# Optimization experiments

Hardware: AMD Instinct MI355X
Metric: run time of the kernel (lower is better)

## Reference

```python
import jax, jax.numpy as jnp
import numpy as np
import math

GROUPS = 32
HEADS = 8
EPS_GN = 1e-5


def group_norm(x, w, b):
    # x: [B, C, H, W]; GroupNorm32 computes in float32
    B, C, H, W = x.shape
    xg = x.astype(jnp.float32).reshape(B, GROUPS, C // GROUPS, H, W)
    mu = xg.mean(axis=(2, 3, 4), keepdims=True)
    var = xg.var(axis=(2, 3, 4), keepdims=True)
    xn = (xg - mu) * jax.lax.rsqrt(var + EPS_GN)
    xn = xn.reshape(B, C, H, W)
    return (xn * w[None, :, None, None] + b[None, :, None, None]).astype(x.dtype)


def fresnel_interference(H, W, wavelength):
    ys, xs = jnp.meshgrid(jnp.arange(H, dtype=jnp.float32),
                          jnp.arange(W, dtype=jnp.float32), indexing='ij')
    pos = jnp.stack([ys, xs], axis=-1).reshape(-1, 2)  # [N, 2]
    diff = pos[None, :, :] - pos[:, None, :]           # [N, N, 2]
    dist = jnp.sqrt((diff ** 2).sum(-1) + 1e-8)        # [N, N]
    phase = 2.0 * math.pi * dist / (jnp.abs(wavelength) * H + 1e-6)
    return jnp.cos(phase)


def fresnel_attn(h, qkv_w, out_w, out_b, wavelength):
    B, C, H, W = h.shape
    N = H * W
    dh = C // HEADS
    scale = dh ** -0.5
    xf = h.reshape(B, C, N).transpose(0, 2, 1)                 # [B, N, C]
    qkv = xf @ qkv_w                                            # [B, N, 3C]
    q, k, v = jnp.split(qkv, 3, axis=-1)
    def heads(t):
        return t.reshape(B, N, HEADS, dh).transpose(0, 2, 1, 3)  # [B, Hh, N, dh]
    q, k, v = heads(q), heads(k), heads(v)
    dots = jnp.einsum('bhnd,bhmd->bhnm', q, k) * scale
    interference = fresnel_interference(H, W, wavelength)       # [N, N]
    dots = dots + interference[None, None] * 0.1
    attn = jax.nn.softmax(dots, axis=-1)
    out = jnp.einsum('bhnm,bhmd->bhnd', attn, v)
    out = out.transpose(0, 2, 1, 3).reshape(B, N, C)
    out = out @ out_w + out_b
    return out.transpose(0, 2, 1).reshape(B, C, H, W)


def cross_attn(h, context, q_w, k_w, v_w, out_w, out_b):
    B, C, H, W = h.shape
    N = H * W
    inner = q_w.shape[1]
    dh = inner // HEADS
    scale = dh ** -0.5
    xf = h.reshape(B, C, N).transpose(0, 2, 1)                 # [B, N, C]
    q = xf @ q_w                                                # [B, N, inner]
    k = context @ k_w                                           # [B, L, inner]
    v = context @ v_w
    L = context.shape[1]
    q = q.reshape(B, N, HEADS, dh).transpose(0, 2, 1, 3)
    k = k.reshape(B, L, HEADS, dh).transpose(0, 2, 1, 3)
    v = v.reshape(B, L, HEADS, dh).transpose(0, 2, 1, 3)
    attn = jax.nn.softmax(jnp.einsum('bhnd,bhld->bhnl', q, k) * scale, axis=-1)
    out = jnp.einsum('bhnl,bhld->bhnd', attn, v)
    out = out.transpose(0, 2, 1, 3).reshape(B, N, inner)
    out = out @ out_w + out_b
    return out.transpose(0, 2, 1).reshape(B, C, H, W)


def setup_inputs() -> dict:
    key = jax.random.key(0)
    ks = jax.random.split(key, 10)
    B, C, H, W = 4, 512, 32, 32
    ctx_len, ctx_dim = 77, 768
    s = lambda d: 1.0 / math.sqrt(d)
    return {
        'x': jax.random.normal(ks[0], (B, C, H, W), jnp.float32),
        'context': jax.random.normal(ks[1], (B, ctx_len, ctx_dim), jnp.float32),
        'gn1_w': jnp.ones((C,), jnp.float32),
        'gn1_b': jnp.zeros((C,), jnp.float32),
        'gn2_w': jnp.ones((C,), jnp.float32),
        'gn2_b': jnp.zeros((C,), jnp.float32),
        'fa_qkv_w': jax.random.normal(ks[2], (C, 3 * C), jnp.float32) * s(C),
        'fa_out_w': jax.random.normal(ks[3], (C, C), jnp.float32) * s(C),
        'fa_out_b': jnp.zeros((C,), jnp.float32),
        'wavelength': jnp.asarray(0.1, jnp.float32),
        'ca_q_w': jax.random.normal(ks[4], (C, 512), jnp.float32) * s(C),
        'ca_k_w': jax.random.normal(ks[5], (ctx_dim, 512), jnp.float32) * s(ctx_dim),
        'ca_v_w': jax.random.normal(ks[6], (ctx_dim, 512), jnp.float32) * s(ctx_dim),
        'ca_out_w': jax.random.normal(ks[7], (512, C), jnp.float32) * s(512),
        'ca_out_b': jnp.zeros((C,), jnp.float32),
    }


def reference(x, context, gn1_w, gn1_b, gn2_w, gn2_b,
              fa_qkv_w, fa_out_w, fa_out_b, wavelength,
              ca_q_w, ca_k_w, ca_v_w, ca_out_w, ca_out_b):
    h = group_norm(x, gn1_w, gn1_b)
    h = fresnel_attn(h, fa_qkv_w, fa_out_w, fa_out_b, wavelength)
    x = x + h
    h = group_norm(x, gn2_w, gn2_b)
    h = cross_attn(h, context, ca_q_w, ca_k_w, ca_v_w, ca_out_w, ca_out_b)
    return x + h
```

## Files before the change

kernel.cpp:

```cpp
#include <hip/hip_runtime.h>
#include <hip/hip_bf16.h>
#include <math.h>

#define B_    4
#define N_    1024
#define L_    77

typedef float f4 __attribute__((ext_vector_type(4)));
typedef short bf8 __attribute__((ext_vector_type(8)));
typedef short s4v __attribute__((ext_vector_type(4)));

#if __has_builtin(__builtin_amdgcn_exp2f)
#define EXP2(x) __builtin_amdgcn_exp2f(x)
#else
#define EXP2(x) exp2f(x)
#endif

__device__ __forceinline__ float fs(short s) {
    unsigned u = ((unsigned)(unsigned short)s) << 16;
    return __builtin_bit_cast(float, u);
}
__device__ __forceinline__ short sf(float f) {
    unsigned u = __builtin_bit_cast(unsigned, f);
    unsigned r = (u + 0x7FFF + ((u >> 16) & 1)) >> 16;
    return (short)r;
}
__device__ __forceinline__ bf8 zero8() { bf8 v; for (int i = 0; i < 8; ++i) v[i] = 0; return v; }
__device__ __forceinline__ f4 zerof4() { f4 v; for (int i = 0; i < 4; ++i) v[i] = 0.f; return v; }

#define MFMA(a, b, c) __builtin_amdgcn_mfma_f32_16x16x32_bf16((a), (b), (c), 0, 0, 0)

__device__ __forceinline__ void wtile(const float* __restrict__ in, short* __restrict__ out,
                                      int K, int J, int tile, int tid, float (*t)[33])
{
    int jt = J >> 5;
    int j0 = (tile % jt) * 32, k0 = (tile / jt) * 32;
    int tx = tid & 31, ty = tid >> 5;
#pragma unroll
    for (int i = 0; i < 4; ++i)
        t[ty + i * 8][tx] = in[(size_t)(k0 + ty + i * 8) * J + j0 + tx];
    __syncthreads();
#pragma unroll
    for (int i = 0; i < 4; ++i)
        out[(size_t)(j0 + ty + i * 8) * K + k0 + tx] = sf(t[tx][ty + i * 8]);
}

__global__ __launch_bounds__(256)
void prep_mega(const float* __restrict__ wl, short* __restrict__ tab,
               const float* __restrict__ qkvw, short* __restrict__ qkvwT,
               const float* __restrict__ faow, short* __restrict__ faowT,
               const float* __restrict__ caqw, short* __restrict__ caqwT,
               const float* __restrict__ cakw, short* __restrict__ cakwT,
               const float* __restrict__ cavw, short* __restrict__ cavwT,
               const float* __restrict__ caow, short* __restrict__ caowT,
               const float* __restrict__ ctx, short* __restrict__ ctxb)
{
    __shared__ float tls[32][33];
    int bid = blockIdx.x, tid = threadIdx.x;
    if (bid < 16) {
        int idx = bid * 256 + tid;
        if (idx < 3969) {
            int i = idx / 63, j = idx - i * 63;
            float dy = (float)(i - 31), dx = (float)(j - 31);
            float dist = sqrtf(dy * dy + dx * dx + 1e-8f);
            float den = fabsf(wl[0]) * 32.0f + 1e-6f;
            tab[idx] = sf(0.1f * cosf(6.283185307179586f * dist / den) * 1.4426950408889634f);
        }
        return;
    }
    bid -= 16;
    if (bid < 768) { wtile(qkvw, qkvwT, 512, 1536, bid, tid, tls); return; }
    bid -= 768;
    if (bid < 256) { wtile(faow, faowT, 512, 512, bid, tid, tls); return; }
    bid -= 256;
    if (bid < 256) { wtile(caqw, caqwT, 512, 512, bid, tid, tls); return; }
    bid -= 256;
    if (bid < 384) { wtile(cakw, cakwT, 768, 512, bid, tid, tls); return; }
    bid -= 384;
    if (bid < 384) { wtile(cavw, cavwT, 768, 512, bid, tid, tls); return; }
    bid -= 384;
    if (bid < 256) { wtile(caow, caowT, 512, 512, bid, tid, tls); return; }
    bid -= 256;
    int base = bid * 1024 + tid * 4;
    float4 v = *(const float4*)(ctx + base);
    s4v o; o[0] = sf(v.x); o[1] = sf(v.y); o[2] = sf(v.z); o[3] = sf(v.w);
    *(s4v*)(ctxb + base) = o;
}

__global__ __launch_bounds__(256)
void gn1_fused(const float* __restrict__ x, const float* __restrict__ w,
               const float* __restrict__ bs, float* __restrict__ xT,
               short* __restrict__ h1b)
{
    int g = blockIdx.x, b = blockIdx.y;
    const float* xb = x + ((size_t)b * 512 + g * 16) * 1024;
    float s = 0.f, ss = 0.f;
    for (int l = threadIdx.x; l < 4096; l += 256) {
        float4 v = *(const float4*)(xb + l * 4);
        s += v.x + v.y + v.z + v.w;
        ss += v.x * v.x + v.y * v.y + v.z * v.z + v.w * v.w;
    }
    for (int off = 32; off; off >>= 1) {
        s  += __shfl_down(s,  off);
        ss += __shfl_down(ss, off);
    }
    __shared__ float sred[8], ssred[8];
    int wid = threadIdx.x >> 6;
    if ((threadIdx.x & 63) == 0) { sred[wid] = s; ssred[wid] = ss; }
    __syncthreads();
    if (threadIdx.x == 0) {
        float S = 0.f, SS = 0.f;
        for (int i = 0; i < 4; ++i) { S += sred[i]; SS += ssred[i]; }
        float mu = S * (1.f / 16384.f);
        float var = SS * (1.f / 16384.f) - mu * mu;
        sred[4] = mu; ssred[4] = rsqrtf(var + 1e-5f);
    }
    __syncthreads();
    float mu = sred[4], rs = ssred[4];

    int c4 = threadIdx.x & 3, nb = threadIdx.x >> 2;
    int c = g * 16 + c4 * 4;
    float4 wv = *(const float4*)(w + c);
    float4 bv = *(const float4*)(bs + c);
    for (int rep = 0; rep < 16; ++rep) {
        int n = rep * 64 + nb;
        float v0 = xb[(size_t)(c4 * 4 + 0) * 1024 + n];
        float v1 = xb[(size_t)(c4 * 4 + 1) * 1024 + n];
        float v2 = xb[(size_t)(c4 * 4 + 2) * 1024 + n];
        float v3 = xb[(size_t)(c4 * 4 + 3) * 1024 + n];
        float4 y;
        y.x = (v0 - mu) * rs * wv.x + bv.x;
        y.y = (v1 - mu) * rs * wv.y + bv.y;
        y.z = (v2 - mu) * rs * wv.z + bv.z;
        y.w = (v3 - mu) * rs * wv.w + bv.w;
        size_t ro = ((size_t)b * 1024 + n) * 512 + c;
        *(float4*)(xT + ro) = y;
        s4v hb; hb[0] = sf(y.x); hb[1] = sf(y.y); hb[2] = sf(y.z); hb[3] = sf(y.w);
        *(s4v*)(h1b + ro) = hb;
    }
}

__global__ __launch_bounds__(256)
void groupnorm_nc(const float* __restrict__ x, const float* __restrict__ w,
                  const float* __restrict__ bs, short* __restrict__ out)
{
    int g = blockIdx.x, b = blockIdx.y;
    const float* xb = x + (size_t)b * 524288 + g * 16;
    short* ob = out + (size_t)b * 524288 + g * 16;
    float s = 0.f, ss = 0.f;
    for (int l = threadIdx.x; l < 4096; l += 256) {
        int n = l >> 2, c4 = l & 3;
        float4 v = *(const float4*)(xb + (size_t)n * 512 + c4 * 4);
        s += v.x + v.y + v.z + v.w;
        ss += v.x * v.x + v.y * v.y + v.z * v.z + v.w * v.w;
    }
    for (int off = 32; off; off >>= 1) {
        s  += __shfl_down(s,  off);
        ss += __shfl_down(ss, off);
    }
    __shared__ float sred[8], ssred[8];
    int wid = threadIdx.x >> 6;
    if ((threadIdx.x & 63) == 0) { sred[wid] = s; ssred[wid] = ss; }
    __syncthreads();
    if (threadIdx.x == 0) {
        float S = 0.f, SS = 0.f;
        for (int i = 0; i < 4; ++i) { S += sred[i]; SS += ssred[i]; }
        float mu = S * (1.f / 16384.f);
        float var = SS * (1.f / 16384.f) - mu * mu;
        sred[4] = mu; ssred[4] = rsqrtf(var + 1e-5f);
    }
    __syncthreads();
    float mu = sred[4], rs = ssred[4];
    for (int l = threadIdx.x; l < 4096; l += 256) {
        int n = l >> 2, c4 = l & 3, c = g * 16 + c4 * 4;
        float4 v = *(const float4*)(xb + (size_t)n * 512 + c4 * 4);
        s4v o;
        o[0] = sf((v.x - mu) * rs * w[c + 0] + bs[c + 0]);
        o[1] = sf((v.y - mu) * rs * w[c + 1] + bs[c + 1]);
        o[2] = sf((v.z - mu) * rs * w[c + 2] + bs[c + 2]);
        o[3] = sf((v.w - mu) * rs * w[c + 3] + bs[c + 3]);
        *(s4v*)(ob + (size_t)n * 512 + c4 * 4) = o;
    }
}

__global__ __launch_bounds__(256)
void transpose_f32(const float* __restrict__ in, float* __restrict__ out, int R, int C)
{
    __shared__ float t[32][33];
    int tx = threadIdx.x & 31, ty = threadIdx.x >> 5;
    int r0 = blockIdx.y * 32, c0 = blockIdx.x * 32;
    size_t bo = (size_t)blockIdx.z * R * C;
#pragma unroll
    for (int i = 0; i < 4; ++i)
        t[ty + i * 8][tx] = in[bo + (size_t)(r0 + ty + i * 8) * C + c0 + tx];
    __syncthreads();
#pragma unroll
    for (int i = 0; i < 4; ++i)
        out[bo + (size_t)(c0 + ty + i * 8) * R + r0 + tx] = t[tx][ty + i * 8];
}

template<int EPI>
__global__ __launch_bounds__(256)
void gemm_mfma(const short* __restrict__ A, const short* __restrict__ Wt,
               const float* __restrict__ bias, const float* __restrict__ res,
               void* __restrict__ outv, int M, int K, int J,
               long aStride, long oStride)
{
    int j0 = blockIdx.x * 128, m0 = blockIdx.y * 128, b = blockIdx.z;
    __shared__ short As[2][128][40];
    __shared__ short Ws[2][128][40];
    int tid = threadIdx.x, w = tid >> 6, lane = tid & 63;
    int lr = lane & 15, lg = lane >> 4;
    int wr = w >> 1, wc = w & 1;
    const short* Ab = A + (size_t)b * aStride;
    int r0 = tid >> 2, c0 = (tid & 3) * 8;
    int r1 = 64 + r0;
    bool gA0 = (m0 + r0) < M, gA1 = (m0 + r1) < M;
    const short* ap0 = Ab + (size_t)(m0 + r0) * K + c0;
    const short* ap1 = Ab + (size_t)(m0 + r1) * K + c0;
    const short* wp0 = Wt + (size_t)(j0 + r0) * K + c0;
    const short* wp1 = Wt + (size_t)(j0 + r1) * K + c0;

    f4 acc[4][4];
#pragma unroll
    for (int i = 0; i < 4; ++i)
#pragma unroll
        for (int j = 0; j < 4; ++j) acc[i][j] = zerof4();

    *(bf8*)&As[0][r0][c0] = gA0 ? *(const bf8*)ap0 : zero8();
    *(bf8*)&As[0][r1][c0] = gA1 ? *(const bf8*)ap1 : zero8();
    *(bf8*)&Ws[0][r0][c0] = *(const bf8*)wp0;
    *(bf8*)&Ws[0][r1][c0] = *(const bf8*)wp1;
    __syncthreads();

    int nk = K >> 5;
    for (int t = 0; t < nk; ++t) {
        int cur = t & 1;
        bool more = (t + 1) < nk;
        bf8 na0, na1, nw0, nw1;
        if (more) {
            int ko = (t + 1) << 5;
            na0 = gA0 ? *(const bf8*)(ap0 + ko) : zero8();
            na1 = gA1 ? *(const bf8*)(ap1 + ko) : zero8();
            nw0 = *(const bf8*)(wp0 + ko);
            nw1 = *(const bf8*)(wp1 + ko);
        }
        bf8 af[4], bfr[4];
#pragma unroll
        for (int fi = 0; fi < 4; ++fi)
            af[fi] = *(const bf8*)&As[cur][wr * 64 + fi * 16 + lr][lg * 8];
#pragma unroll
        for (int fj = 0; fj < 4; ++fj)
            bfr[fj] = *(const bf8*)&Ws[cur][wc * 64 + fj * 16 + lr][lg * 8];
#pragma unroll
        for (int fi = 0; fi < 4; ++fi)
#pragma unroll
            for (int fj = 0; fj < 4; ++fj)
                acc[fi][fj] = MFMA(af[fi], bfr[fj], acc[fi][fj]);
        if (more) {
            int nb = cur ^ 1;
            *(bf8*)&As[nb][r0][c0] = na0;
            *(bf8*)&As[nb][r1][c0] = na1;
            *(bf8*)&Ws[nb][r0][c0] = nw0;
            *(bf8*)&Ws[nb][r1][c0] = nw1;
        }
        __syncthreads();
    }

    if (EPI == 0) {
        short* out = (short*)outv + (size_t)b * oStride;
#pragma unroll
        for (int fi = 0; fi < 4; ++fi)
#pragma unroll
            for (int reg = 0; reg < 4; ++reg) {
                int m = m0 + wr * 64 + fi * 16 + lg * 4 + reg;
                if (m < M) {
#pragma unroll
                    for (int fj = 0; fj < 4; ++fj)
                        out[(size_t)m * J + j0 + wc * 64 + fj * 16 + lr] = sf(acc[fi][fj][reg]);
                }
            }
    } else {
        float* out = (float*)outv + (size_t)b * oStride;
        const float* rp = res + (size_t)b * oStride;
        float bv[4];
#pragma unroll
        for (int fj = 0; fj < 4; ++fj) bv[fj] = bias[j0 + wc * 64 + fj * 16 + lr];
#pragma unroll
        for (int fi = 0; fi < 4; ++fi)
#pragma unroll
            for (int reg = 0; reg < 4; ++reg) {
                int m = m0 + wr * 64 + fi * 16 + lg * 4 + reg;
                size_t ro = (size_t)m * J + j0 + wc * 64;
#pragma unroll
                for (int fj = 0; fj < 4; ++fj) {
                    size_t idx = ro + fj * 16 + lr;
                    out[idx] = acc[fi][fj][reg] + bv[fj] + rp[idx];
                }
            }
    }
}

__global__ __launch_bounds__(256)
void vhead_t(const short* __restrict__ src, short* __restrict__ dst,
             int Nsrc, int Jfull, int cb, int Np)
{
    int n0 = blockIdx.x * 64, h = blockIdx.y, b = blockIdx.z;
    __shared__ short t[64][72];
    int tid = threadIdx.x;
    for (int l = tid; l < 512; l += 256) {
        int n = l >> 3, dq = l & 7;
        bf8 v = zero8();
        if (n0 + n < Nsrc)
            v = *(const bf8*)(src + ((size_t)b * Nsrc + n0 + n) * Jfull + cb + h * 64 + dq * 8);
        *(bf8*)&t[n][dq * 8] = v;
    }
    __syncthreads();
    for (int l = tid; l < 512; l += 256) {
        int d = l >> 3, nq = l & 7;
        if (n0 + nq * 8 < Np) {
            bf8 v;
#pragma unroll
            for (int i = 0; i < 8; ++i) {
                int j = (i + nq) & 7;
                v[j] = t[nq * 8 + j][d];
            }
            *(bf8*)(dst + (((size_t)(b * 8 + h)) * 64 + d) * Np + n0 + nq * 8) = v;
        }
    }
}

__global__ __launch_bounds__(256)
void fresnel_attn_v2(const short* __restrict__ qkv, const short* __restrict__ Vg,
                     const short* __restrict__ tab, short* __restrict__ ao)
{
    int qb = blockIdx.x, h = blockIdx.y, b = blockIdx.z;
    int n0 = qb * 64;
    __shared__ short Ks[2][64][64];
    __shared__ short Vt[2][64][64];
    __shared__ short Ps[4][16][72];
    __shared__ short tabs[3969];
    int tid = threadIdx.x, w = tid >> 6, lane = tid & 63;
    int lr = lane & 15, lg = lane >> 4;
    const short* qp = qkv + (size_t)b * N_ * 1536;
    const short* vp = Vg + ((size_t)(b * 8 + h)) * 65536;

    for (int l = tid; l < 3969; l += 256) tabs[l] = tab[l];

    int q = n0 + w * 16 + lr;
    bf8 qf0 = *(const bf8*)(qp + (size_t)q * 1536 + h * 64 + lg * 8);
    bf8 qf1 = *(const bf8*)(qp + (size_t)q * 1536 + h * 64 + 32 + lg * 8);

    int sr0 = tid >> 3, sc0 = tid & 7;
    int sr1 = 32 + sr0;
    int sw0 = ((sc0 ^ (sr0 & 7))) * 8;
    int sw1 = ((sc0 ^ (sr1 & 7))) * 8;

    *(bf8*)&Ks[0][sr0][sw0] = *(const bf8*)(qp + (size_t)sr0 * 1536 + 512 + h * 64 + sc0 * 8);
    *(bf8*)&Ks[0][sr1][sw1] = *(const bf8*)(qp + (size_t)sr1 * 1536 + 512 + h * 64 + sc0 * 8);
    *(bf8*)&Vt[0][sr0][sw0] = *(const bf8*)(vp + (size_t)sr0 * 1024 + sc0 * 8);
    *(bf8*)&Vt[0][sr1][sw1] = *(const bf8*)(vp + (size_t)sr1 * 1024 + sc0 * 8);
    __syncthreads();

    float mrun = -1e30f, lrun = 0.f;
    f4 o[4];
#pragma unroll
    for (int i = 0; i < 4; ++i) o[i] = zerof4();

    int ybase = (q >> 5) + 31;
    int xbase = (q & 31) + 31 - lg * 4;
    int rsw = lr & 7;
    int rc0 = (lg ^ rsw) * 8;
    int rc1 = ((4 + lg) ^ rsw) * 8;

    for (int t = 0; t < 16; ++t) {
        int cur = t & 1;
        int m0 = t << 6;
        bool more = t < 15;
        bf8 nk0, nk1, nv0, nv1;
        if (more) {
            int m1 = m0 + 64;
            nk0 = *(const bf8*)(qp + (size_t)(m1 + sr0) * 1536 + 512 + h * 64 + sc0 * 8);
            nk1 = *(const bf8*)(qp + (size_t)(m1 + sr1) * 1536 + 512 + h * 64 + sc0 * 8);
            nv0 = *(const bf8*)(vp + (size_t)sr0 * 1024 + m1 + sc0 * 8);
            nv1 = *(const bf8*)(vp + (size_t)sr1 * 1024 + m1 + sc0 * 8);
        }

        f4 sa[4];
#pragma unroll
        for (int fj = 0; fj < 4; ++fj) sa[fj] = zerof4();
#pragma unroll
        for (int fj = 0; fj < 4; ++fj)
            sa[fj] = MFMA(*(const bf8*)&Ks[cur][fj * 16 + lr][rc0], qf0, sa[fj]);
#pragma unroll
        for (int fj = 0; fj < 4; ++fj)
            sa[fj] = MFMA(*(const bf8*)&Ks[cur][fj * 16 + lr][rc1], qf1, sa[fj]);

        int yb = ybase - (m0 >> 5);
        float pv[4][4];
        float tmax = -1e30f;
#pragma unroll
        for (int fj = 0; fj < 4; ++fj) {
            int rowoff = (yb - (fj >> 1)) * 63 + xbase - (fj & 1) * 16;
#pragma unroll
            for (int reg = 0; reg < 4; ++reg) {
                float t2 = fmaf(sa[fj][reg], 0.18033688011112042f, fs(tabs[rowoff - reg]));
                pv[fj][reg] = t2;
                tmax = fmaxf(tmax, t2);
            }
        }
        tmax = fmaxf(tmax, __shfl_xor(tmax, 16));
        tmax = fmaxf(tmax, __shfl_xor(tmax, 32));
        float mnew = fmaxf(mrun, tmax);
        float rsc = EXP2(mrun - mnew);
        mrun = mnew;
        float psum = 0.f;
#pragma unroll
        for (int fj = 0; fj < 4; ++fj) {
            s4v pw;
#pragma unroll
            for (int reg = 0; reg < 4; ++reg) {
                float p = EXP2(pv[fj][reg] - mnew);
                psum += p;
                pw[reg] = sf(p);
            }
            *(s4v*)&Ps[w][lr][fj * 16 + lg * 4] = pw;
        }
        psum += __shfl_xor(psum, 16);
        psum += __shfl_xor(psum, 32);
        lrun = lrun * rsc + psum;
#pragma unroll
        for (int fd = 0; fd < 4; ++fd)
#pragma unroll
            for (int reg = 0; reg < 4; ++reg) o[fd][reg] *= rsc;

        bf8 pa0 = *(const bf8*)&Ps[w][lr][lg * 8];
        bf8 pa1 = *(const bf8*)&Ps[w][lr][32 + lg * 8];
#pragma unroll
        for (int fd = 0; fd < 4; ++fd) {
            o[fd] = MFMA(*(const bf8*)&Vt[cur][fd * 16 + lr][rc0], pa0, o[fd]);
            o[fd] = MFMA(*(const bf8*)&Vt[cur][fd * 16 + lr][rc1], pa1, o[fd]);
        }

        if (more) {
            int nb = cur ^ 1;
            *(bf8*)&Ks[nb][sr0][sw0] = nk0;
            *(bf8*)&Ks[nb][sr1][sw1] = nk1;
            *(bf8*)&Vt[nb][sr0][sw0] = nv0;
            *(bf8*)&Vt[nb][sr1][sw1] = nv1;
        }
        __syncthreads();
    }

    float inv = 1.f / lrun;
    size_t rb = ((size_t)b * N_ + q) * 512 + h * 64;
#pragma unroll
    for (int fd = 0; fd < 4; ++fd) {
        s4v ov;
#pragma unroll
        for (int reg = 0; reg < 4; ++reg) ov[reg] = sf(o[fd][reg] * inv);
        *(s4v*)(ao + rb + fd * 16 + lg * 4) = ov;
    }
}

__global__ __launch_bounds__(256)
void cross_attn_mfma(const short* __restrict__ q2, const short* __restrict__ kv,
                     const short* __restrict__ v2t, short* __restrict__ ao2)
{
    int qb = blockIdx.x, h = blockIdx.y, b = blockIdx.z;
    int n0 = qb * 64;
    __shared__ short Qs[64][72], Ks[96][72], Vt[64][104];
    __shared__ short Ps[4][16][104];
    int tid = threadIdx.x, w = tid >> 6, lane = tid & 63;
    int lr = lane & 15, lg = lane >> 4;

    for (int l = tid; l < 512; l += 256) {
        int n = l >> 3, dq = l & 7;
        *(bf8*)&Qs[n][dq * 8] = *(const bf8*)(q2 + ((size_t)b * N_ + n0 + n) * 512 + h * 64 + dq * 8);
    }
    for (int l = tid; l < 768; l += 256) {
        int m = l >> 3, dq = l & 7;
        bf8 v = zero8();
        if (m < L_) v = *(const bf8*)(kv + ((size_t)b * L_ + m) * 1024 + h * 64 + dq * 8);
        *(bf8*)&Ks[m][dq * 8] = v;
    }
    for (int l = tid; l < 768; l += 256) {
        int d = l / 12, cq = l % 12;
        bf8 v = zero8();
        if (cq < 10) v = *(const bf8*)(v2t + (((size_t)(b * 8 + h)) * 64 + d) * 80 + cq * 8);
        *(bf8*)&Vt[d][cq * 8] = v;
    }
    __syncthreads();

    f4 sacc[6];
#pragma unroll
    for (int fj = 0; fj < 6; ++fj) sacc[fj] = zerof4();
#pragma unroll
    for (int kc = 0; kc < 2; ++kc) {
        bf8 aq = *(const bf8*)&Qs[w * 16 + lr][kc * 32 + lg * 8];
#pragma unroll
        for (int fj = 0; fj < 6; ++fj)
            sacc[fj] = MFMA(aq, *(const bf8*)&Ks[fj * 16 + lr][kc * 32 + lg * 8], sacc[fj]);
    }

    float rinv[4];
#pragma unroll
    for (int reg = 0; reg < 4; ++reg) {
        float sv[6];
#pragma unroll
        for (int fj = 0; fj < 6; ++fj) {
            int m = fj * 16 + lr;
            sv[fj] = (m < L_) ? sacc[fj][reg] * 0.125f : -30000.f;
        }
        float mx = sv[0];
#pragma unroll
        for (int fj = 1; fj < 6; ++fj) mx = fmaxf(mx, sv[fj]);
#pragma unroll
        for (int off = 1; off < 16; off <<= 1) mx = fmaxf(mx, __shfl_xor(mx, off));
        float psum = 0.f;
#pragma unroll
        for (int fj = 0; fj < 6; ++fj) {
            float p = __expf(sv[fj] - mx);
            psum += p;
            Ps[w][lg * 4 + reg][fj * 16 + lr] = sf(p);
        }
#pragma unroll
        for (int off = 1; off < 16; off <<= 1) psum += __shfl_xor(psum, off);
        rinv[reg] = 1.f / psum;
    }
    __syncthreads();

    f4 o[4];
#pragma unroll
    for (int fd = 0; fd < 4; ++fd) o[fd] = zerof4();
#pragma unroll
    for (int kc = 0; kc < 3; ++kc) {
        bf8 ap = *(const bf8*)&Ps[w][lr][kc * 32 + lg * 8];
#pragma unroll
        for (int fd = 0; fd < 4; ++fd)
            o[fd] = MFMA(ap, *(const bf8*)&Vt[fd * 16 + lr][kc * 32 + lg * 8], o[fd]);
    }

#pragma unroll
    for (int reg = 0; reg < 4; ++reg) {
        size_t rb = ((size_t)b * N_ + n0 + w * 16 + lg * 4 + reg) * 512 + h * 64;
#pragma unroll
        for (int fd = 0; fd < 4; ++fd)
            ao2[rb + fd * 16 + lr] = sf(o[fd][reg] * rinv[reg]);
    }
}

extern "C" void kernel_launch(void* const* d_in, const int* in_sizes, int n_in,
                              void* d_out, int out_size, void* d_ws, size_t ws_size,
                              hipStream_t stream)
{
    const float* x    = (const float*)d_in[0];
    const float* ctx  = (const float*)d_in[1];
    const float* gn1w = (const float*)d_in[2];
    const float* gn1b = (const float*)d_in[3];
    const float* gn2w = (const float*)d_in[4];
    const float* gn2b = (const float*)d_in[5];
    const float* qkvw = (const float*)d_in[6];
    const float* faow = (const float*)d_in[7];
    const float* faob = (const float*)d_in[8];
    const float* wl   = (const float*)d_in[9];
    const float* caqw = (const float*)d_in[10];
    const float* cakw = (const float*)d_in[11];
    const float* cavw = (const float*)d_in[12];
    const float* caow = (const float*)d_in[13];
    const float* caob = (const float*)d_in[14];
    float* out = (float*)d_out;
    char* ws = (char*)d_ws;

    float* xT     = (float*)(ws + 0);
    float* x1T    = (float*)(ws + 8388608);
    short* qkvb   = (short*)(ws + 16777216);
    float* finalT = (float*)(ws + 16777216);
    short* Vg     = (short*)(ws + 29360128);
    short* h1b    = (short*)(ws + 33554432);
    short* ao     = (short*)(ws + 37748736);
    short* q2b    = (short*)(ws + 41943040);
    short* qkvwT  = (short*)(ws + 46137344);
    short* faowT  = (short*)(ws + 47710208);
    short* caqwT  = (short*)(ws + 48234496);
    short* cakwT  = (short*)(ws + 48758784);
    short* cavwT  = (short*)(ws + 49545216);
    short* caowT  = (short*)(ws + 50331648);
    short* kv2b   = (short*)(ws + 50855936);
    short* v2t    = (short*)(ws + 51486720);
    short* ctxb   = (short*)(ws + 51814400);
    short* tab    = (short*)(ws + 52287488);

    prep_mega<<<2551, 256, 0, stream>>>(wl, tab, qkvw, qkvwT, faow, faowT,
                                        caqw, caqwT, cakw, cakwT, cavw, cavwT,
                                        caow, caowT, ctx, ctxb);
    gn1_fused<<<dim3(32, 4), 256, 0, stream>>>(x, gn1w, gn1b, xT, h1b);
    gemm_mfma<0><<<dim3(12, 8, 4), 256, 0, stream>>>(
        h1b, qkvwT, nullptr, nullptr, qkvb, 1024, 512, 1536, 524288L, 1572864L);
    vhead_t<<<dim3(16, 8, 4), 256, 0, stream>>>(qkvb, Vg, 1024, 1536, 1024, 1024);
    fresnel_attn_v2<<<dim3(16, 8, 4), 256, 0, stream>>>(qkvb, Vg, tab, ao);
    gemm_mfma<1><<<dim3(4, 8, 4), 256, 0, stream>>>(
        ao, faowT, faob, xT, x1T, 1024, 512, 512, 524288L, 524288L);
    groupnorm_nc<<<dim3(32, 4), 256, 0, stream>>>(x1T, gn2w, gn2b, h1b);
    gemm_mfma<0><<<dim3(4, 8, 4), 256, 0, stream>>>(
        h1b, caqwT, nullptr, nullptr, q2b, 1024, 512, 512, 524288L, 524288L);
    gemm_mfma<0><<<dim3(8, 1, 4), 256, 0, stream>>>(
        ctxb, cakwT, nullptr, nullptr, kv2b, 77, 768, 1024, 59136L, 78848L);
    vhead_t<<<dim3(2, 8, 4), 256, 0, stream>>>(kv2b, v2t, 77, 1024, 512, 80);
    cross_attn_mfma<<<dim3(16, 8, 4), 256, 0, stream>>>(q2b, kv2b, v2t, ao);
    gemm_mfma<1><<<dim3(4, 8, 4), 256, 0, stream>>>(
        ao, caowT, caob, x1T, finalT, 1024, 512, 512, 524288L, 524288L);
    transpose_f32<<<dim3(16, 32, 4), 256, 0, stream>>>(finalT, out, 1024, 512);
}
```

Before: 242.5 us.

## Keep residual stream in NCHW layout and fuse V-transposes into GEMM epilogues

Switches the output projections to compute the transposed product (weights as A, activations as B), so the residual adds and the final output stay in channel-major layout. This removes the final f32 transpose kernel and the fp32 transposed copies of x. The QKV and context K/V GEMMs get new epilogues that write V directly in head-transposed layout, which removes both vhead_t launches. The cost is strided 8-byte epilogue stores in place of the separate transpose passes, plus a second GroupNorm kernel that reads channel-major input.

```diff
diff --git a/kernel.cpp b/kernel.cpp
--- a/kernel.cpp
+++ b/kernel.cpp
@@ -88,12 +88,11 @@
 }
 
 __global__ __launch_bounds__(256)
-void gn1_fused(const float* __restrict__ x, const float* __restrict__ w,
-               const float* __restrict__ bs, float* __restrict__ xT,
-               short* __restrict__ h1b)
+void gn_fused(const float* __restrict__ src, const float* __restrict__ w,
+              const float* __restrict__ bs, short* __restrict__ dst)
 {
     int g = blockIdx.x, b = blockIdx.y;
-    const float* xb = x + ((size_t)b * 512 + g * 16) * 1024;
+    const float* xb = src + ((size_t)b * 512 + g * 16) * 1024;
     float s = 0.f, ss = 0.f;
     for (int l = threadIdx.x; l < 4096; l += 256) {
         float4 v = *(const float4*)(xb + l * 4);
@@ -128,83 +127,22 @@
         float v1 = xb[(size_t)(c4 * 4 + 1) * 1024 + n];
         float v2 = xb[(size_t)(c4 * 4 + 2) * 1024 + n];
         float v3 = xb[(size_t)(c4 * 4 + 3) * 1024 + n];
-        float4 y;
-        y.x = (v0 - mu) * rs * wv.x + bv.x;
-        y.y = (v1 - mu) * rs * wv.y + bv.y;
-        y.z = (v2 - mu) * rs * wv.z + bv.z;
-        y.w = (v3 - mu) * rs * wv.w + bv.w;
-        size_t ro = ((size_t)b * 1024 + n) * 512 + c;
-        *(float4*)(xT + ro) = y;
-        s4v hb; hb[0] = sf(y.x); hb[1] = sf(y.y); hb[2] = sf(y.z); hb[3] = sf(y.w);
-        *(s4v*)(h1b + ro) = hb;
-    }
-}
-
-__global__ __launch_bounds__(256)
-void groupnorm_nc(const float* __restrict__ x, const float* __restrict__ w,
-                  const float* __restrict__ bs, short* __restrict__ out)
-{
-    int g = blockIdx.x, b = blockIdx.y;
-    const float* xb = x + (size_t)b * 524288 + g * 16;
-    short* ob = out + (size_t)b * 524288 + g * 16;
-    float s = 0.f, ss = 0.f;
-    for (int l = threadIdx.x; l < 4096; l += 256) {
-        int n = l >> 2, c4 = l & 3;
-        float4 v = *(const float4*)(xb + (size_t)n * 512 + c4 * 4);
-        s += v.x + v.y + v.z + v.w;
-        ss += v.x * v.x + v.y * v.y + v.z * v.z + v.w * v.w;
-    }
-    for (int off = 32; off; off >>= 1) {
-        s  += __shfl_down(s,  off);
-        ss += __shfl_down(ss, off);
-    }
-    __shared__ float sred[8], ssred[8];
-    int wid = threadIdx.x >> 6;
-    if ((threadIdx.x & 63) == 0) { sred[wid] = s; ssred[wid] = ss; }
-    __syncthreads();
-    if (threadIdx.x == 0) {
-        float S = 0.f, SS = 0.f;
-        for (int i = 0; i < 4; ++i) { S += sred[i]; SS += ssred[i]; }
-        float mu = S * (1.f / 16384.f);
-        float var = SS * (1.f / 16384.f) - mu * mu;
-        sred[4] = mu; ssred[4] = rsqrtf(var + 1e-5f);
-    }
-    __syncthreads();
-    float mu = sred[4], rs = ssred[4];
-    for (int l = threadIdx.x; l < 4096; l += 256) {
-        int n = l >> 2, c4 = l & 3, c = g * 16 + c4 * 4;
-        float4 v = *(const float4*)(xb + (size_t)n * 512 + c4 * 4);
-        s4v o;
-        o[0] = sf((v.x - mu) * rs * w[c + 0] + bs[c + 0]);
-        o[1] = sf((v.y - mu) * rs * w[c + 1] + bs[c + 1]);
-        o[2] = sf((v.z - mu) * rs * w[c + 2] + bs[c + 2]);
-        o[3] = sf((v.w - mu) * rs * w[c + 3] + bs[c + 3]);
-        *(s4v*)(ob + (size_t)n * 512 + c4 * 4) = o;
-    }
-}
-
-__global__ __launch_bounds__(256)
-void transpose_f32(const float* __restrict__ in, float* __restrict__ out, int R, int C)
-{
-    __shared__ float t[32][33];
-    int tx = threadIdx.x & 31, ty = threadIdx.x >> 5;
-    int r0 = blockIdx.y * 32, c0 = blockIdx.x * 32;
-    size_t bo = (size_t)blockIdx.z * R * C;
-#pragma unroll
-    for (int i = 0; i < 4; ++i)
-        t[ty + i * 8][tx] = in[bo + (size_t)(r0 + ty + i * 8) * C + c0 + tx];
-    __syncthreads();
-#pragma unroll
-    for (int i = 0; i < 4; ++i)
-        out[bo + (size_t)(c0 + ty + i * 8) * R + r0 + tx] = t[tx][ty + i * 8];
+        s4v hb;
+        hb[0] = sf((v0 - mu) * rs * wv.x + bv.x);
+        hb[1] = sf((v1 - mu) * rs * wv.y + bv.y);
+        hb[2] = sf((v2 - mu) * rs * wv.z + bv.z);
+        hb[3] = sf((v3 - mu) * rs * wv.w + bv.w);
+        *(s4v*)(dst + ((size_t)b * 1024 + n) * 512 + c) = hb;
+    }
 }
 
 template<int EPI>
 __global__ __launch_bounds__(256)
 void gemm_mfma(const short* __restrict__ A, const short* __restrict__ Wt,
                const float* __restrict__ bias, const float* __restrict__ res,
-               void* __restrict__ outv, int M, int K, int J,
-               long aStride, long oStride)
+               void* __restrict__ outv, void* __restrict__ out2v,
+               int M, int K, int J,
+               long aStride, long wStride, long oStride, long o2Stride)
 {
     int j0 = blockIdx.x * 128, m0 = blockIdx.y * 128, b = blockIdx.z;
     __shared__ short As[2][128][40];
@@ -212,14 +150,15 @@
     int tid = threadIdx.x, w = tid >> 6, lane = tid & 63;
     int lr = lane & 15, lg = lane >> 4;
     int wr = w >> 1, wc = w & 1;
-    const short* Ab = A + (size_t)b * aStride;
+    const short* Ab  = A  + (size_t)b * aStride;
+    const short* Wtb = Wt + (size_t)b * wStride;
     int r0 = tid >> 2, c0 = (tid & 3) * 8;
     int r1 = 64 + r0;
     bool gA0 = (m0 + r0) < M, gA1 = (m0 + r1) < M;
     const short* ap0 = Ab + (size_t)(m0 + r0) * K + c0;
     const short* ap1 = Ab + (size_t)(m0 + r1) * K + c0;
-    const short* wp0 = Wt + (size_t)(j0 + r0) * K + c0;
-    const short* wp1 = Wt + (size_t)(j0 + r1) * K + c0;
+    const short* wp0 = Wtb + (size_t)(j0 + r0) * K + c0;
+    const short* wp1 = Wtb + (size_t)(j0 + r1) * K + c0;
 
     f4 acc[4][4];
 #pragma unroll
@@ -280,14 +219,13 @@
                         out[(size_t)m * J + j0 + wc * 64 + fj * 16 + lr] = sf(acc[fi][fj][reg]);
                 }
             }
-    } else {
+    } else if (EPI == 1) {
         float* out = (float*)outv + (size_t)b * oStride;
         const float* rp = res + (size_t)b * oStride;
-        float bv[4];
-#pragma unroll
-        for (int fj = 0; fj < 4; ++fj) bv[fj] = bias[j0 + wc * 64 + fj * 16 + lr];
-#pragma unroll
-        for (int fi = 0; fi < 4; ++fi)
+#pragma unroll
+        for (int fi = 0; fi < 4; ++fi) {
+            float4 bq = *(const float4*)(bias + m0 + wr * 64 + fi * 16 + lg * 4);
+            float bvr[4] = {bq.x, bq.y, bq.z, bq.w};
 #pragma unroll
             for (int reg = 0; reg < 4; ++reg) {
                 int m = m0 + wr * 64 + fi * 16 + lg * 4 + reg;
@@ -295,43 +233,73 @@
 #pragma unroll
                 for (int fj = 0; fj < 4; ++fj) {
                     size_t idx = ro + fj * 16 + lr;
-                    out[idx] = acc[fi][fj][reg] + bv[fj] + rp[idx];
+                    out[idx] = acc[fi][fj][reg] + bvr[reg] + rp[idx];
                 }
             }
+        }
+    } else if (EPI == 3) {
+        if (j0 < 1024) {
+            short* out = (short*)outv + (size_t)b * oStride;
+#pragma unroll
+            for (int fi = 0; fi < 4; ++fi)
+#pragma unroll
+                for (int reg = 0; reg < 4; ++reg) {
+                    int m = m0 + wr * 64 + fi * 16 + lg * 4 + reg;
+#pragma unroll
+                    for (int fj = 0; fj < 4; ++fj)
+                        out[(size_t)m * 1024 + j0 + wc * 64 + fj * 16 + lr] = sf(acc[fi][fj][reg]);
+                }
+        } else {
+            short* Vg = (short*)out2v + (size_t)b * o2Stride;
+#pragma unroll
+            for (int fi = 0; fi < 4; ++fi) {
+                int n = m0 + wr * 64 + fi * 16 + lg * 4;
+#pragma unroll
+                for (int fj = 0; fj < 4; ++fj) {
+                    int dg = j0 - 1024 + wc * 64 + fj * 16 + lr;
+                    s4v v;
+#pragma unroll
+                    for (int reg = 0; reg < 4; ++reg) v[reg] = sf(acc[fi][fj][reg]);
+                    *(s4v*)(Vg + (size_t)dg * 1024 + n) = v;
+                }
+            }
+        }
+    } else {
+        if (j0 < 512) {
+            short* out = (short*)outv + (size_t)b * oStride;
+#pragma unroll
+            for (int fi = 0; fi < 4; ++fi)
+#pragma unroll
+                for (int reg = 0; reg < 4; ++reg) {
+                    int m = m0 + wr * 64 + fi * 16 + lg * 4 + reg;
+                    if (m < M) {
+#pragma unroll
+                        for (int fj = 0; fj < 4; ++fj)
+                            out[(size_t)m * 512 + j0 + wc * 64 + fj * 16 + lr] = sf(acc[fi][fj][reg]);
+                    }
+                }
+        } else {
+            short* vt = (short*)out2v + (size_t)b * o2Stride;
+#pragma unroll
+            for (int fi = 0; fi < 4; ++fi) {
+                int l0 = wr * 64 + fi * 16 + lg * 4;
+                if (l0 < 80) {
+#pragma unroll
+                    for (int fj = 0; fj < 4; ++fj) {
+                        int dg = j0 - 512 + wc * 64 + fj * 16 + lr;
+                        s4v v;
+#pragma unroll
+                        for (int reg = 0; reg < 4; ++reg) v[reg] = sf(acc[fi][fj][reg]);
+                        *(s4v*)(vt + (size_t)dg * 80 + l0) = v;
+                    }
+                }
+            }
+        }
     }
 }
 
 __global__ __launch_bounds__(256)
-void vhead_t(const short* __restrict__ src, short* __restrict__ dst,
-             int Nsrc, int Jfull, int cb, int Np)
-{
-    int n0 = blockIdx.x * 64, h = blockIdx.y, b = blockIdx.z;
-    __shared__ short t[64][72];
-    int tid = threadIdx.x;
-    for (int l = tid; l < 512; l += 256) {
-        int n = l >> 3, dq = l & 7;
-        bf8 v = zero8();
-        if (n0 + n < Nsrc)
-            v = *(const bf8*)(src + ((size_t)b * Nsrc + n0 + n) * Jfull + cb + h * 64 + dq * 8);
-        *(bf8*)&t[n][dq * 8] = v;
-    }
-    __syncthreads();
-    for (int l = tid; l < 512; l += 256) {
-        int d = l >> 3, nq = l & 7;
-        if (n0 + nq * 8 < Np) {
-            bf8 v;
-#pragma unroll
-            for (int i = 0; i < 8; ++i) {
-                int j = (i + nq) & 7;
-                v[j] = t[nq * 8 + j][d];
-            }
-            *(bf8*)(dst + (((size_t)(b * 8 + h)) * 64 + d) * Np + n0 + nq * 8) = v;
-        }
-    }
-}
-
-__global__ __launch_bounds__(256)
-void fresnel_attn_v2(const short* __restrict__ qkv, const short* __restrict__ Vg,
+void fresnel_attn_v2(const short* __restrict__ qkb, const short* __restrict__ Vg,
                      const short* __restrict__ tab, short* __restrict__ ao)
 {
     int qb = blockIdx.x, h = blockIdx.y, b = blockIdx.z;
@@ -339,25 +307,26 @@
     __shared__ short Ks[2][64][64];
     __shared__ short Vt[2][64][64];
     __shared__ short Ps[4][16][72];
-    __shared__ short tabs[3969];
+    __shared__ short tabs[4032];
     int tid = threadIdx.x, w = tid >> 6, lane = tid & 63;
     int lr = lane & 15, lg = lane >> 4;
-    const short* qp = qkv + (size_t)b * N_ * 1536;
-    const short* vp = Vg + ((size_t)(b * 8 + h)) * 65536;
-
-    for (int l = tid; l < 3969; l += 256) tabs[l] = tab[l];
+    const short* qp = qkb + (size_t)b * 1048576;
+    const short* vp = Vg + ((size_t)b * 512 + h * 64) * 1024;
+
+    for (int l = tid; l < 504; l += 256)
+        *(bf8*)&tabs[l * 8] = *(const bf8*)(tab + l * 8);
 
     int q = n0 + w * 16 + lr;
-    bf8 qf0 = *(const bf8*)(qp + (size_t)q * 1536 + h * 64 + lg * 8);
-    bf8 qf1 = *(const bf8*)(qp + (size_t)q * 1536 + h * 64 + 32 + lg * 8);
+    bf8 qf0 = *(const bf8*)(qp + (size_t)q * 1024 + h * 64 + lg * 8);
+    bf8 qf1 = *(const bf8*)(qp + (size_t)q * 1024 + h * 64 + 32 + lg * 8);
 
     int sr0 = tid >> 3, sc0 = tid & 7;
     int sr1 = 32 + sr0;
     int sw0 = ((sc0 ^ (sr0 & 7))) * 8;
     int sw1 = ((sc0 ^ (sr1 & 7))) * 8;
 
-    *(bf8*)&Ks[0][sr0][sw0] = *(const bf8*)(qp + (size_t)sr0 * 1536 + 512 + h * 64 + sc0 * 8);
-    *(bf8*)&Ks[0][sr1][sw1] = *(const bf8*)(qp + (size_t)sr1 * 1536 + 512 + h * 64 + sc0 * 8);
+    *(bf8*)&Ks[0][sr0][sw0] = *(const bf8*)(qp + (size_t)sr0 * 1024 + 512 + h * 64 + sc0 * 8);
+    *(bf8*)&Ks[0][sr1][sw1] = *(const bf8*)(qp + (size_t)sr1 * 1024 + 512 + h * 64 + sc0 * 8);
     *(bf8*)&Vt[0][sr0][sw0] = *(const bf8*)(vp + (size_t)sr0 * 1024 + sc0 * 8);
     *(bf8*)&Vt[0][sr1][sw1] = *(const bf8*)(vp + (size_t)sr1 * 1024 + sc0 * 8);
     __syncthreads();
@@ -380,8 +349,8 @@
         bf8 nk0, nk1, nv0, nv1;
         if (more) {
             int m1 = m0 + 64;
-            nk0 = *(const bf8*)(qp + (size_t)(m1 + sr0) * 1536 + 512 + h * 64 + sc0 * 8);
-            nk1 = *(const bf8*)(qp + (size_t)(m1 + sr1) * 1536 + 512 + h * 64 + sc0 * 8);
+            nk0 = *(const bf8*)(qp + (size_t)(m1 + sr0) * 1024 + 512 + h * 64 + sc0 * 8);
+            nk1 = *(const bf8*)(qp + (size_t)(m1 + sr1) * 1024 + 512 + h * 64 + sc0 * 8);
             nv0 = *(const bf8*)(vp + (size_t)sr0 * 1024 + m1 + sc0 * 8);
             nv1 = *(const bf8*)(vp + (size_t)sr1 * 1024 + m1 + sc0 * 8);
         }
@@ -464,7 +433,7 @@
 }
 
 __global__ __launch_bounds__(256)
-void cross_attn_mfma(const short* __restrict__ q2, const short* __restrict__ kv,
+void cross_attn_mfma(const short* __restrict__ q2, const short* __restrict__ k2,
                      const short* __restrict__ v2t, short* __restrict__ ao2)
 {
     int qb = blockIdx.x, h = blockIdx.y, b = blockIdx.z;
@@ -481,13 +450,13 @@
     for (int l = tid; l < 768; l += 256) {
         int m = l >> 3, dq = l & 7;
         bf8 v = zero8();
-        if (m < L_) v = *(const bf8*)(kv + ((size_t)b * L_ + m) * 1024 + h * 64 + dq * 8);
+        if (m < L_) v = *(const bf8*)(k2 + ((size_t)b * L_ + m) * 512 + h * 64 + dq * 8);
         *(bf8*)&Ks[m][dq * 8] = v;
     }
     for (int l = tid; l < 768; l += 256) {
         int d = l / 12, cq = l % 12;
         bf8 v = zero8();
-        if (cq < 10) v = *(const bf8*)(v2t + (((size_t)(b * 8 + h)) * 64 + d) * 80 + cq * 8);
+        if (cq < 10) v = *(const bf8*)(v2t + ((size_t)b * 512 + h * 64 + d) * 80 + cq * 8);
         *(bf8*)&Vt[d][cq * 8] = v;
     }
     __syncthreads();
@@ -572,43 +541,43 @@
     float* out = (float*)d_out;
     char* ws = (char*)d_ws;
 
-    float* xT     = (float*)(ws + 0);
-    float* x1T    = (float*)(ws + 8388608);
-    short* qkvb   = (short*)(ws + 16777216);
-    float* finalT = (float*)(ws + 16777216);
-    short* Vg     = (short*)(ws + 29360128);
-    short* h1b    = (short*)(ws + 33554432);
-    short* ao     = (short*)(ws + 37748736);
-    short* q2b    = (short*)(ws + 41943040);
-    short* qkvwT  = (short*)(ws + 46137344);
-    short* faowT  = (short*)(ws + 47710208);
-    short* caqwT  = (short*)(ws + 48234496);
-    short* cakwT  = (short*)(ws + 48758784);
-    short* cavwT  = (short*)(ws + 49545216);
-    short* caowT  = (short*)(ws + 50331648);
-    short* kv2b   = (short*)(ws + 50855936);
-    short* v2t    = (short*)(ws + 51486720);
-    short* ctxb   = (short*)(ws + 51814400);
-    short* tab    = (short*)(ws + 52287488);
+    float* x1    = (float*)(ws + 0);
+    short* qkb   = (short*)(ws + 8388608);
+    short* Vg    = (short*)(ws + 16777216);
+    short* h1b   = (short*)(ws + 20971520);
+    short* ao    = (short*)(ws + 25165824);
+    short* q2b   = (short*)(ws + 29360128);
+    short* qkvwT = (short*)(ws + 33554432);
+    short* faowT = (short*)(ws + 35127296);
+    short* caqwT = (short*)(ws + 35651584);
+    short* cakwT = (short*)(ws + 36175872);
+    short* cavwT = (short*)(ws + 36962304);
+    short* caowT = (short*)(ws + 37748736);
+    short* k2b   = (short*)(ws + 38273024);
+    short* v2t   = (short*)(ws + 38588416);
+    short* ctxb  = (short*)(ws + 38916096);
+    short* tab   = (short*)(ws + 39389184);
 
     prep_mega<<<2551, 256, 0, stream>>>(wl, tab, qkvw, qkvwT, faow, faowT,
                                         caqw, caqwT, cakw, cakwT, cavw, cavwT,
                                         caow, caowT, ctx, ctxb);
-    gn1_fused<<<dim3(32, 4), 256, 0, stream>>>(x, gn1w, gn1b, xT, h1b);
-    gemm_mfma<0><<<dim3(12, 8, 4), 256, 0, stream>>>(
-        h1b, qkvwT, nullptr, nullptr, qkvb, 1024, 512, 1536, 524288L, 1572864L);
-    vhead_t<<<dim3(16, 8, 4), 256, 0, stream>>>(qkvb, Vg, 1024, 1536, 1024, 1024);
-    fresnel_attn_v2<<<dim3(16, 8, 4), 256, 0, stream>>>(qkvb, Vg, tab, ao);
-    gemm_mfma<1><<<dim3(4, 8, 4), 256, 0, stream>>>(
-        ao, faowT, faob, xT, x1T, 1024, 512, 512, 524288L, 524288L);
-    groupnorm_nc<<<dim3(32, 4), 256, 0, stream>>>(x1T, gn2w, gn2b, h1b);
+    gn_fused<<<dim3(32, 4), 256, 0, stream>>>(x, gn1w, gn1b, h1b);
+    gemm_mfma<3><<<dim3(12, 8, 4), 256, 0, stream>>>(
+        h1b, qkvwT, nullptr, nullptr, qkb, Vg, 1024, 512, 1536,
+        524288L, 0L, 1048576L, 524288L);
+    fresnel_attn_v2<<<dim3(16, 8, 4), 256, 0, stream>>>(qkb, Vg, tab, ao);
+    gemm_mfma<1><<<dim3(8, 4, 4), 256, 0, stream>>>(
+        faowT, ao, faob, x, x1, nullptr, 512, 512, 1024,
+        0L, 524288L, 524288L, 0L);
+    gn_fused<<<dim3(32, 4), 256, 0, stream>>>(x1, gn2w, gn2b, h1b);
     gemm_mfma<0><<<dim3(4, 8, 4), 256, 0, stream>>>(
-        h1b, caqwT, nullptr, nullptr, q2b, 1024, 512, 512, 524288L, 524288L);
-    gemm_mfma<0><<<dim3(8, 1, 4), 256, 0, stream>>>(
-        ctxb, cakwT, nullptr, nullptr, kv2b, 77, 768, 1024, 59136L, 78848L);
-    vhead_t<<<dim3(2, 8, 4), 256, 0, stream>>>(kv2b, v2t, 77, 1024, 512, 80);
-    cross_attn_mfma<<<dim3(16, 8, 4), 256, 0, stream>>>(q2b, kv2b, v2t, ao);
-    gemm_mfma<1><<<dim3(4, 8, 4), 256, 0, stream>>>(
-        ao, caowT, caob, x1T, finalT, 1024, 512, 512, 524288L, 524288L);
-    transpose_f32<<<dim3(16, 32, 4), 256, 0, stream>>>(finalT, out, 1024, 512);
-}
+        h1b, caqwT, nullptr, nullptr, q2b, nullptr, 1024, 512, 512,
+        524288L, 0L, 524288L, 0L);
+    gemm_mfma<4><<<dim3(8, 1, 4), 256, 0, stream>>>(
+        ctxb, cakwT, nullptr, nullptr, k2b, v2t, 77, 768, 1024,
+        59136L, 0L, 39424L, 40960L);
+    cross_attn_mfma<<<dim3(16, 8, 4), 256, 0, stream>>>(q2b, k2b, v2t, ao);
+    gemm_mfma<1><<<dim3(8, 4, 4), 256, 0, stream>>>(
+        caowT, ao, caob, x1, out, nullptr, 512, 512, 1024,
+        0L, 524288L, 524288L, 0L);
+}
```

New measurement: 223.3 us. -7.9%, faster.
